# Optimization experiments

Hardware: AMD Instinct MI355X
Metric: run time of the kernel (lower is better)

Reference implementation:

```python
import jax, jax.numpy as jnp
import numpy as np
from jax import lax

B, C, H, W = 8, 64, 96, 96
OC = 64
KH = KW = 3
DG = 1
STRIDE = 1
PAD = 1
DIL = 1


def setup_inputs() -> dict:
    key = jax.random.key(0)
    k1, k2, k3, k4, k5 = jax.random.split(key, 5)
    x = jax.random.normal(k1, (B, C, H, W), jnp.float32)
    off_ch = DG * 3 * KH * KW
    # small random offset/mask conv params (the original inits them to zero,
    # which would make offsets degenerate; small values exercise the sampler)
    w_off = jax.random.normal(k2, (off_ch, C, KH, KW), jnp.float32) * 0.01
    b_off = jax.random.normal(k3, (off_ch,), jnp.float32) * 0.01
    stdv = 1.0 / float(np.sqrt(C * KH * KW))
    weight = jax.random.uniform(k4, (OC, C, KH, KW), jnp.float32, -stdv, stdv)
    bias = jax.random.uniform(k5, (OC,), jnp.float32, -stdv, stdv)
    return {"x": x, "w_off": w_off, "b_off": b_off, "weight": weight, "bias": bias}


def _deform_conv(x, w_off, b_off, weight, bias):
    Bt, Ct, Ht, Wt = x.shape
    K = KH * KW
    # standard conv producing offsets + mask logits
    om = lax.conv_general_dilated(
        x, w_off, (STRIDE, STRIDE), ((PAD, PAD), (PAD, PAD)),
        rhs_dilation=(DIL, DIL), dimension_numbers=("NCHW", "OIHW", "NCHW"),
    ) + b_off[None, :, None, None]
    o1, o2, m = jnp.split(om, 3, axis=1)  # each [B, DG*K, Ho, Wo]
    Ho, Wo = o1.shape[2], o1.shape[3]
    mask = jax.nn.sigmoid(m).reshape(Bt, DG, 1, K, Ho, Wo)
    off_y = o1.reshape(Bt, DG, K, Ho, Wo)
    off_x = o2.reshape(Bt, DG, K, Ho, Wo)
    # base sampling grid: p = out_pos*stride - pad + k*dilation + offset
    kk = jnp.arange(K)
    base_y = (kk // KW)[:, None] * DIL + (jnp.arange(Ho) * STRIDE - PAD)[None, :]  # [K, Ho]
    base_x = (kk % KW)[:, None] * DIL + (jnp.arange(Wo) * STRIDE - PAD)[None, :]   # [K, Wo]
    py = off_y + base_y[None, None, :, :, None].astype(x.dtype)  # [B, DG, K, Ho, Wo]
    px = off_x + base_x[None, None, :, None, :].astype(x.dtype)
    y0 = jnp.floor(py)
    x0 = jnp.floor(px)
    ly = py - y0
    lx = px - x0
    Cg = Ct // DG
    xg = x.reshape(Bt, DG, Cg, Ht * Wt)

    def gath(xf, idx):  # xf [Cg, H*W], idx [K*Ho*Wo]
        return jnp.take(xf, idx, axis=1)

    gather = jax.vmap(jax.vmap(gath))  # over B, DG

    sampled = jnp.zeros((Bt, DG, Cg, K, Ho, Wo), x.dtype)
    for dy, dx, wgt in ((0, 0, (1 - ly) * (1 - lx)), (0, 1, (1 - ly) * lx),
                        (1, 0, ly * (1 - lx)), (1, 1, ly * lx)):
        yy = y0 + dy
        xx = x0 + dx
        valid = (yy >= 0) & (yy < Ht) & (xx >= 0) & (xx < Wt)
        yi = jnp.clip(yy, 0, Ht - 1).astype(jnp.int32)
        xi = jnp.clip(xx, 0, Wt - 1).astype(jnp.int32)
        idx = (yi * Wt + xi).reshape(Bt, DG, K * Ho * Wo)
        v = gather(xg, idx).reshape(Bt, DG, Cg, K, Ho, Wo)
        sampled = sampled + v * (wgt * valid)[:, :, None]
    sampled = sampled * mask  # modulated
    wr = weight.reshape(OC, DG, Cg, K)
    out = jnp.einsum("bgckhw,ogck->bohw", sampled, wr) + bias[None, :, None, None]
    return out


def reference(x, w_off, b_off, weight, bias):
    return _deform_conv(x, w_off, b_off, weight, bias)
```

## Files before the change

### kernel.cpp

```cpp
#include <hip/hip_runtime.h>
#include <math.h>

#define Bn 8
#define Cn 64
#define Hn 96
#define Wn 96
#define HWn (Hn*Wn)
#define OCn 64
#define Kn 9
#define OFFCn 27
#define NPIX (Bn*HWn)
#define PGRPS (NPIX/64)

#define WS_DWORDS (45*NPIX)
#define WS_BYTES  ((size_t)WS_DWORDS*4)

__global__ __launch_bounds__(256, 2) void dcn_k1(
    const float* __restrict__ x,
    const float* __restrict__ w_off,
    const float* __restrict__ b_off,
    float* __restrict__ pwbuf,
    int*   __restrict__ abuf)
{
    __shared__ float lds[4 * 64 * OFFCn];

    const int tid  = threadIdx.x;
    const int lane = tid & 63;
    const int wv   = tid >> 6;
    const int cbase = __builtin_amdgcn_readfirstlane(wv * 16);

    const int p  = blockIdx.x * 64 + lane;
    const int b  = p / HWn;
    const int hw = p % HWn;
    const int ho = hw / Wn;
    const int wo = hw % Wn;

    const float* xb = x + b * (Cn * HWn);

    int   toff[Kn];
    float tval[Kn];
#pragma unroll
    for (int ki = 0; ki < Kn; ++ki) {
        const int yy = ho + ki / 3 - 1, xx = wo + ki % 3 - 1;
        const bool v = (yy >= 0) && (yy < Hn) && (xx >= 0) && (xx < Wn);
        toff[ki] = min(max(yy, 0), Hn - 1) * Wn + min(max(xx, 0), Wn - 1);
        tval[ki] = v ? 1.0f : 0.0f;
    }

    float om[OFFCn];
#pragma unroll
    for (int j = 0; j < OFFCn; ++j) om[j] = 0.0f;

    for (int ci = 0; ci < 16; ++ci) {
        const int c = cbase + ci;
        const float* xc = xb + c * HWn;
        float xk[Kn];
#pragma unroll
        for (int ki = 0; ki < Kn; ++ki)
            xk[ki] = xc[toff[ki]] * tval[ki];

        const float* wc = w_off + c * Kn;
#pragma unroll
        for (int och = 0; och < OFFCn; ++och) {
            const float* wp = wc + och * (Cn * Kn);
            float a = om[och];
#pragma unroll
            for (int ki = 0; ki < Kn; ++ki)
                a = fmaf(xk[ki], wp[ki], a);
            om[och] = a;
        }
    }

#pragma unroll
    for (int j = 0; j < OFFCn; ++j)
        lds[(wv * 64 + lane) * OFFCn + j] = om[j];
    __syncthreads();
#pragma unroll
    for (int j = 0; j < OFFCn; ++j) {
        float a = b_off[j];
#pragma unroll
        for (int ww = 0; ww < 4; ++ww)
            a += lds[(ww * 64 + lane) * OFFCn + j];
        om[j] = a;
    }

    float pw0[Kn], pw1[Kn], pw2[Kn], pw3[Kn];
    int   pav[Kn];
#pragma unroll
    for (int ki = 0; ki < Kn; ++ki) {
        const float py = om[ki]      + (float)(ki / 3 + ho - 1);
        const float px = om[Kn + ki] + (float)(ki % 3 + wo - 1);
        const float m  = 1.0f / (1.0f + __expf(-om[2 * Kn + ki]));

        const float y0f = floorf(py), x0f = floorf(px);
        const float ly = py - y0f, lx = px - x0f;
        const int iy0 = (int)y0f, ix0 = (int)x0f;
        const int iy1 = iy0 + 1,  ix1 = ix0 + 1;

        const float vy0 = (iy0 >= 0 && iy0 < Hn) ? 1.0f : 0.0f;
        const float vy1 = (iy1 >= 0 && iy1 < Hn) ? 1.0f : 0.0f;
        const float vx0 = (ix0 >= 0 && ix0 < Wn) ? 1.0f : 0.0f;
        const float vx1 = (ix1 >= 0 && ix1 < Wn) ? 1.0f : 0.0f;

        const int iy0c = min(max(iy0, 0), Hn - 1);
        const int iy1c = min(max(iy1, 0), Hn - 1);
        const int ix0c = min(max(ix0, 0), Wn - 1);
        const int ix1c = min(max(ix1, 0), Wn - 1);

        pw0[ki] = m * (1.0f - ly) * (1.0f - lx) * vy0 * vx0;
        pw1[ki] = m * (1.0f - ly) * lx          * vy0 * vx1;
        pw2[ki] = m * ly          * (1.0f - lx) * vy1 * vx0;
        pw3[ki] = m * ly          * lx          * vy1 * vx1;
        const int pa  = iy0c * Wn + ix0c;
        const int dx  = ix1c - ix0c;
        const int dyw = (iy1c - iy0c) * Wn;
        pav[ki] = pa | (dx << 16) | (dyw << 17);
    }

    if (wv == 0) {
#pragma unroll
        for (int ki = 0; ki < Kn; ++ki) pwbuf[(0 * Kn + ki) * NPIX + p] = pw0[ki];
#pragma unroll
        for (int ki = 0; ki < Kn; ++ki) abuf[ki * NPIX + p] = pav[ki];
    } else if (wv == 1) {
#pragma unroll
        for (int ki = 0; ki < Kn; ++ki) pwbuf[(1 * Kn + ki) * NPIX + p] = pw1[ki];
    } else if (wv == 2) {
#pragma unroll
        for (int ki = 0; ki < Kn; ++ki) pwbuf[(2 * Kn + ki) * NPIX + p] = pw2[ki];
    } else {
#pragma unroll
        for (int ki = 0; ki < Kn; ++ki) pwbuf[(3 * Kn + ki) * NPIX + p] = pw3[ki];
    }
}

__global__ __launch_bounds__(512, 4) void dcn_k2(
    const float* __restrict__ x,
    const float* __restrict__ weight,
    const float* __restrict__ bias,
    const float* __restrict__ pwbuf,
    const int*   __restrict__ abuf,
    float* __restrict__ out)
{
    __shared__ float smp[8 * Kn * 64];

    const int tid  = threadIdx.x;
    const int lane = tid & 63;
    const int wv   = tid >> 6;
    const int ocb  = __builtin_amdgcn_readfirstlane(wv * 8);

    const int p  = blockIdx.x * 64 + lane;
    const int b  = p / HWn;
    const int hw = p % HWn;

    const float* xb = x + b * (Cn * HWn);

    float pw0[Kn], pw1[Kn], pw2[Kn], pw3[Kn];
    int   pav[Kn];
#pragma unroll
    for (int ki = 0; ki < Kn; ++ki) pw0[ki] = pwbuf[(0 * Kn + ki) * NPIX + p];
#pragma unroll
    for (int ki = 0; ki < Kn; ++ki) pw1[ki] = pwbuf[(1 * Kn + ki) * NPIX + p];
#pragma unroll
    for (int ki = 0; ki < Kn; ++ki) pw2[ki] = pwbuf[(2 * Kn + ki) * NPIX + p];
#pragma unroll
    for (int ki = 0; ki < Kn; ++ki) pw3[ki] = pwbuf[(3 * Kn + ki) * NPIX + p];
#pragma unroll
    for (int ki = 0; ki < Kn; ++ki) pav[ki] = abuf[ki * NPIX + p];

    float acc[8];
#pragma unroll
    for (int j = 0; j < 8; ++j) acc[j] = bias[ocb + j];

    for (int ch = 0; ch < 8; ++ch) {
        {
            const float* xc = xb + (ch * 8 + wv) * HWn;
#pragma unroll
            for (int ki = 0; ki < Kn; ++ki) {
                const int av  = pav[ki];
                const int pa  = av & 0xFFFF;
                const int dx  = (av >> 16) & 1;
                const int dyw = av >> 17;
                const float* bp = xc + pa;
                const float v00 = bp[0];
                const float v01 = bp[dx];
                const float v10 = bp[dyw];
                const float v11 = bp[dyw + dx];
                smp[(wv * Kn + ki) * 64 + lane] =
                    pw0[ki] * v00 + pw1[ki] * v01 + pw2[ki] * v10 + pw3[ki] * v11;
            }
        }
        __syncthreads();

        const float* wch = weight + (ocb * Cn + ch * 8) * Kn;
#pragma unroll 2
        for (int c8 = 0; c8 < 8; ++c8) {
            float sv[Kn];
#pragma unroll
            for (int ki = 0; ki < Kn; ++ki)
                sv[ki] = smp[(c8 * Kn + ki) * 64 + lane];
#pragma unroll
            for (int j = 0; j < 8; ++j) {
                const float* wp = wch + j * (Cn * Kn) + c8 * Kn;
                float a = acc[j];
#pragma unroll
                for (int ki = 0; ki < Kn; ++ki)
                    a = fmaf(sv[ki], wp[ki], a);
                acc[j] = a;
            }
        }
        __syncthreads();
    }

    float* ob = out + b * (OCn * HWn) + hw;
#pragma unroll
    for (int j = 0; j < 8; ++j)
        ob[(ocb + j) * HWn] = acc[j];
}

__global__ __launch_bounds__(64) void dcn_r1(
    const float* __restrict__ x,
    const float* __restrict__ w_off,
    const float* __restrict__ b_off,
    const float* __restrict__ weight,
    const float* __restrict__ bias,
    float* __restrict__ out)
{
    const int p  = blockIdx.x * 64 + threadIdx.x;
    const int b  = p / HWn;
    const int hw = p % HWn;
    const int ho = hw / Wn;
    const int wo = hw % Wn;
    const float* xb = x + b * (Cn * HWn);

    float om[OFFCn];
#pragma unroll
    for (int j = 0; j < OFFCn; ++j) om[j] = b_off[j];

    int   toff[Kn];
    float tval[Kn];
#pragma unroll
    for (int ki = 0; ki < Kn; ++ki) {
        const int yy = ho + ki / 3 - 1, xx = wo + ki % 3 - 1;
        const bool v = (yy >= 0) && (yy < Hn) && (xx >= 0) && (xx < Wn);
        toff[ki] = min(max(yy, 0), Hn - 1) * Wn + min(max(xx, 0), Wn - 1);
        tval[ki] = v ? 1.0f : 0.0f;
    }
    for (int c = 0; c < Cn; ++c) {
        const float* xc = xb + c * HWn;
        float xk[Kn];
#pragma unroll
        for (int ki = 0; ki < Kn; ++ki) xk[ki] = xc[toff[ki]] * tval[ki];
        const float* wc = w_off + c * Kn;
#pragma unroll
        for (int och = 0; och < OFFCn; ++och) {
            const float* wp = wc + och * (Cn * Kn);
            float a = om[och];
#pragma unroll
            for (int ki = 0; ki < Kn; ++ki) a = fmaf(xk[ki], wp[ki], a);
            om[och] = a;
        }
    }
    float pw0[Kn], pw1[Kn], pw2[Kn], pw3[Kn];
    int   pa[Kn], pdx[Kn], pdyw[Kn];
#pragma unroll
    for (int ki = 0; ki < Kn; ++ki) {
        const float py = om[ki]      + (float)(ki / 3 + ho - 1);
        const float px = om[Kn + ki] + (float)(ki % 3 + wo - 1);
        const float m  = 1.0f / (1.0f + __expf(-om[2 * Kn + ki]));
        const float y0f = floorf(py), x0f = floorf(px);
        const float ly = py - y0f, lx = px - x0f;
        const int iy0 = (int)y0f, ix0 = (int)x0f;
        const int iy1 = iy0 + 1,  ix1 = ix0 + 1;
        const float vy0 = (iy0 >= 0 && iy0 < Hn) ? 1.0f : 0.0f;
        const float vy1 = (iy1 >= 0 && iy1 < Hn) ? 1.0f : 0.0f;
        const float vx0 = (ix0 >= 0 && ix0 < Wn) ? 1.0f : 0.0f;
        const float vx1 = (ix1 >= 0 && ix1 < Wn) ? 1.0f : 0.0f;
        const int iy0c = min(max(iy0, 0), Hn - 1);
        const int iy1c = min(max(iy1, 0), Hn - 1);
        const int ix0c = min(max(ix0, 0), Wn - 1);
        const int ix1c = min(max(ix1, 0), Wn - 1);
        pw0[ki] = m * (1.0f - ly) * (1.0f - lx) * vy0 * vx0;
        pw1[ki] = m * (1.0f - ly) * lx          * vy0 * vx1;
        pw2[ki] = m * ly          * (1.0f - lx) * vy1 * vx0;
        pw3[ki] = m * ly          * lx          * vy1 * vx1;
        pa[ki]   = iy0c * Wn + ix0c;
        pdx[ki]  = ix1c - ix0c;
        pdyw[ki] = (iy1c - iy0c) * Wn;
    }
    float acc[OCn];
#pragma unroll
    for (int oc = 0; oc < OCn; ++oc) acc[oc] = bias[oc];
    for (int c = 0; c < Cn; ++c) {
        const float* xc = xb + c * HWn;
        float s[Kn];
#pragma unroll
        for (int ki = 0; ki < Kn; ++ki) {
            const float* bp = xc + pa[ki];
            s[ki] = pw0[ki] * bp[0] + pw1[ki] * bp[pdx[ki]]
                  + pw2[ki] * bp[pdyw[ki]] + pw3[ki] * bp[pdyw[ki] + pdx[ki]];
        }
        const float* wc = weight + c * Kn;
#pragma unroll
        for (int oc = 0; oc < OCn; ++oc) {
            const float* wp = wc + oc * (Cn * Kn);
            float a = acc[oc];
#pragma unroll
            for (int ki = 0; ki < Kn; ++ki) a = fmaf(s[ki], wp[ki], a);
            acc[oc] = a;
        }
    }
    float* ob = out + b * (OCn * HWn) + hw;
#pragma unroll
    for (int oc = 0; oc < OCn; ++oc) ob[oc * HWn] = acc[oc];
}

extern "C" void kernel_launch(void* const* d_in, const int* in_sizes, int n_in,
                              void* d_out, int out_size, void* d_ws, size_t ws_size,
                              hipStream_t stream) {
    const float* x      = (const float*)d_in[0];
    const float* w_off  = (const float*)d_in[1];
    const float* b_off  = (const float*)d_in[2];
    const float* weight = (const float*)d_in[3];
    const float* bias   = (const float*)d_in[4];
    float* out = (float*)d_out;

    if (ws_size >= WS_BYTES) {
        float* pwbuf = (float*)d_ws;
        int*   abuf  = (int*)((float*)d_ws + 36 * NPIX);
        hipLaunchKernelGGL(dcn_k1, dim3(PGRPS), dim3(256), 0, stream,
                           x, w_off, b_off, pwbuf, abuf);
        hipLaunchKernelGGL(dcn_k2, dim3(PGRPS), dim3(512), 0, stream,
                           x, weight, bias, pwbuf, abuf, out);
    } else {
        hipLaunchKernelGGL(dcn_r1, dim3(NPIX / 64), dim3(64), 0, stream,
                           x, w_off, b_off, weight, bias, out);
    }
}
```

Baseline: 283.4 us.

## Move deformable conv GEMM onto bf16 MFMA with split-precision sampled values

Replaces the scalar FMA loop that contracts sampled values against the weights with MFMA 16x16x32 bf16 matrix instructions. A new prep kernel packs the weights into bf16 fragment layout, padded to K=160 per 16-channel chunk. Sampled values are split into high and low bf16 halves, computed on two wave planes, and summed through LDS at the end to keep accuracy close to fp32. The aim is to remove the large VALU FMA cost of the contraction. The trade-offs are an extra launch, padding work, and weights carried only at bf16 precision.

```diff
diff --git a/kernel.cpp b/kernel.cpp
--- a/kernel.cpp
+++ b/kernel.cpp
@@ -12,8 +12,44 @@
 #define NPIX (Bn*HWn)
 #define PGRPS (NPIX/64)
 
-#define WS_DWORDS (45*NPIX)
-#define WS_BYTES  ((size_t)WS_DWORDS*4)
+#define WS_PARAM_DWORDS (45*NPIX)
+#define WPACK_SHORTS (4*20*64*8)
+#define WS_BYTES ((size_t)WS_PARAM_DWORDS*4 + (size_t)WPACK_SHORTS*2)
+
+typedef __attribute__((ext_vector_type(8))) short short8v;
+typedef __attribute__((ext_vector_type(4))) float f32x4;
+
+static __device__ __forceinline__ unsigned short bf16_rne(float f) {
+    unsigned int b = __float_as_uint(f);
+    return (unsigned short)((b + 0x7FFFu + ((b >> 16) & 1u)) >> 16);
+}
+static __device__ __forceinline__ float bf16_back(unsigned short h) {
+    return __uint_as_float(((unsigned int)h) << 16);
+}
+
+__global__ __launch_bounds__(512) void dcn_wprep(
+    const float* __restrict__ weight, short* __restrict__ wpack)
+{
+    const int g = blockIdx.x * 512 + threadIdx.x;
+    const int oct = g / 1280;
+    const int rem = g - oct * 1280;
+    const int gks = rem >> 6;
+    const int l   = rem & 63;
+    const int chunk = gks / 5;
+    const int kk    = (gks % 5) * 32 + ((l >> 4) & 3) * 8;
+    const int oc    = oct * 16 + (l & 15);
+
+    short8v v;
+    if (kk < 144) {
+        const float* src = weight + oc * 576 + chunk * 144 + kk;
+#pragma unroll
+        for (int j = 0; j < 8; ++j) v[j] = (short)bf16_rne(src[j]);
+    } else {
+#pragma unroll
+        for (int j = 0; j < 8; ++j) v[j] = 0;
+    }
+    ((short8v*)wpack)[g] = v;
+}
 
 __global__ __launch_bounds__(256, 2) void dcn_k1(
     const float* __restrict__ x,
@@ -134,24 +170,28 @@
     }
 }
 
+#define SMP_PITCH 66
+#define SMP_U16   (160 * SMP_PITCH)
 __global__ __launch_bounds__(512, 4) void dcn_k2(
     const float* __restrict__ x,
-    const float* __restrict__ weight,
+    const short* __restrict__ wpack,
     const float* __restrict__ bias,
     const float* __restrict__ pwbuf,
     const int*   __restrict__ abuf,
     float* __restrict__ out)
 {
-    __shared__ float smp[8 * Kn * 64];
+    __shared__ unsigned short smp[2 * SMP_U16];
 
     const int tid  = threadIdx.x;
     const int lane = tid & 63;
-    const int wv   = tid >> 6;
-    const int ocb  = __builtin_amdgcn_readfirstlane(wv * 8);
-
-    const int p  = blockIdx.x * 64 + lane;
-    const int b  = p / HWn;
-    const int hw = p % HWn;
+    const int w    = tid >> 6;
+    const int pxt  = w & 3;
+    const int plane= w >> 2;
+
+    const int p0  = blockIdx.x * 64;
+    const int b   = p0 / HWn;
+    const int hwb = p0 % HWn;
+    const int p   = p0 + lane;
 
     const float* xb = x + b * (Cn * HWn);
 
@@ -168,13 +208,26 @@
 #pragma unroll
     for (int ki = 0; ki < Kn; ++ki) pav[ki] = abuf[ki * NPIX + p];
 
-    float acc[8];
-#pragma unroll
-    for (int j = 0; j < 8; ++j) acc[j] = bias[ocb + j];
-
-    for (int ch = 0; ch < 8; ++ch) {
-        {
-            const float* xc = xb + (ch * 8 + wv) * HWn;
+    {
+        unsigned int* zh = (unsigned int*)(smp + 144 * SMP_PITCH);
+        unsigned int* zl = (unsigned int*)(smp + SMP_U16 + 144 * SMP_PITCH);
+        for (int idx = tid; idx < (16 * SMP_PITCH) / 2; idx += 512) {
+            zh[idx] = 0u; zl[idx] = 0u;
+        }
+    }
+
+    f32x4 acc[4];
+#pragma unroll
+    for (int oct = 0; oct < 4; ++oct) acc[oct] = (f32x4){0.f, 0.f, 0.f, 0.f};
+
+    unsigned short* smpP = smp + plane * SMP_U16;
+    const short8v* wfrag = (const short8v*)wpack;
+
+    for (int chunk = 0; chunk < 4; ++chunk) {
+#pragma unroll
+        for (int cc = 0; cc < 2; ++cc) {
+            const int cin = (w << 1) | cc;
+            const float* xc = xb + (chunk * 16 + cin) * HWn;
 #pragma unroll
             for (int ki = 0; ki < Kn; ++ki) {
                 const int av  = pav[ki];
@@ -182,40 +235,63 @@
                 const int dx  = (av >> 16) & 1;
                 const int dyw = av >> 17;
                 const float* bp = xc + pa;
-                const float v00 = bp[0];
-                const float v01 = bp[dx];
-                const float v10 = bp[dyw];
-                const float v11 = bp[dyw + dx];
-                smp[(wv * Kn + ki) * 64 + lane] =
-                    pw0[ki] * v00 + pw1[ki] * v01 + pw2[ki] * v10 + pw3[ki] * v11;
+                const float v = pw0[ki] * bp[0] + pw1[ki] * bp[dx]
+                              + pw2[ki] * bp[dyw] + pw3[ki] * bp[dyw + dx];
+                const unsigned short hb = bf16_rne(v);
+                const unsigned short lb = bf16_rne(v - bf16_back(hb));
+                const int k = cin * Kn + ki;
+                smp[k * SMP_PITCH + lane]            = hb;
+                smp[SMP_U16 + k * SMP_PITCH + lane]  = lb;
             }
         }
         __syncthreads();
 
-        const float* wch = weight + (ocb * Cn + ch * 8) * Kn;
-#pragma unroll 2
-        for (int c8 = 0; c8 < 8; ++c8) {
-            float sv[Kn];
-#pragma unroll
-            for (int ki = 0; ki < Kn; ++ki)
-                sv[ki] = smp[(c8 * Kn + ki) * 64 + lane];
-#pragma unroll
-            for (int j = 0; j < 8; ++j) {
-                const float* wp = wch + j * (Cn * Kn) + c8 * Kn;
-                float a = acc[j];
-#pragma unroll
-                for (int ki = 0; ki < Kn; ++ki)
-                    a = fmaf(sv[ki], wp[ki], a);
-                acc[j] = a;
+#pragma unroll
+        for (int ks = 0; ks < 5; ++ks) {
+            short8v av0 = wfrag[((0 * 20) + chunk * 5 + ks) * 64 + lane];
+            short8v av1 = wfrag[((1 * 20) + chunk * 5 + ks) * 64 + lane];
+            short8v av2 = wfrag[((2 * 20) + chunk * 5 + ks) * 64 + lane];
+            short8v av3 = wfrag[((3 * 20) + chunk * 5 + ks) * 64 + lane];
+
+            short8v bv;
+            const int kb = ks * 32 + ((lane >> 4) & 3) * 8;
+            const int pxl = pxt * 16 + (lane & 15);
+#pragma unroll
+            for (int j = 0; j < 8; ++j)
+                bv[j] = (short)smpP[(kb + j) * SMP_PITCH + pxl];
+
+            acc[0] = __builtin_amdgcn_mfma_f32_16x16x32_bf16(av0, bv, acc[0], 0, 0, 0);
+            acc[1] = __builtin_amdgcn_mfma_f32_16x16x32_bf16(av1, bv, acc[1], 0, 0, 0);
+            acc[2] = __builtin_amdgcn_mfma_f32_16x16x32_bf16(av2, bv, acc[2], 0, 0, 0);
+            acc[3] = __builtin_amdgcn_mfma_f32_16x16x32_bf16(av3, bv, acc[3], 0, 0, 0);
+        }
+        __syncthreads();
+    }
+
+    float* cred = (float*)smp;
+    const int rbase = ((lane >> 4) & 3) * 4;
+    const int pxl   = pxt * 16 + (lane & 15);
+    if (plane == 1) {
+#pragma unroll
+        for (int oct = 0; oct < 4; ++oct)
+#pragma unroll
+            for (int r = 0; r < 4; ++r)
+                cred[(oct * 16 + rbase + r) * SMP_PITCH + pxl] = acc[oct][r];
+    }
+    __syncthreads();
+    if (plane == 0) {
+        float* ob = out + b * (OCn * HWn) + hwb + pxl;
+#pragma unroll
+        for (int oct = 0; oct < 4; ++oct) {
+#pragma unroll
+            for (int r = 0; r < 4; ++r) {
+                const int oc = oct * 16 + rbase + r;
+                const float v = acc[oct][r]
+                              + cred[oc * SMP_PITCH + pxl] + bias[oc];
+                ob[oc * HWn] = v;
             }
         }
-        __syncthreads();
-    }
-
-    float* ob = out + b * (OCn * HWn) + hw;
-#pragma unroll
-    for (int j = 0; j < 8; ++j)
-        ob[(ocb + j) * HWn] = acc[j];
+    }
 }
 
 __global__ __launch_bounds__(64) void dcn_r1(
@@ -328,10 +404,13 @@
     if (ws_size >= WS_BYTES) {
         float* pwbuf = (float*)d_ws;
         int*   abuf  = (int*)((float*)d_ws + 36 * NPIX);
+        short* wpack = (short*)((float*)d_ws + WS_PARAM_DWORDS);
+        hipLaunchKernelGGL(dcn_wprep, dim3(10), dim3(512), 0, stream,
+                           weight, wpack);
         hipLaunchKernelGGL(dcn_k1, dim3(PGRPS), dim3(256), 0, stream,
                            x, w_off, b_off, pwbuf, abuf);
         hipLaunchKernelGGL(dcn_k2, dim3(PGRPS), dim3(512), 0, stream,
-                           x, weight, bias, pwbuf, abuf, out);
+                           x, wpack, bias, pwbuf, abuf, out);
     } else {
         hipLaunchKernelGGL(dcn_r1, dim3(NPIX / 64), dim3(64), 0, stream,
                            x, w_off, b_off, weight, bias, out);
```

New measurement: 418.8 us. +47.8%, slower.

## Convert both kernels to persistent grids with atomic work-stealing over pixel groups

Applied to the files above, without the earlier changes.

Both stages now launch a fixed grid of 1024 blocks that repeatedly pull 64-pixel groups from global atomic counters, which a new tiny kernel zeroes first. The aim is to cut block launch and scheduling overhead and to balance load across CUs. dcn_k1's launch bounds also rise from 2 to 4 blocks per SM to raise occupancy. The cost is an extra kernel launch, one atomic plus a barrier per group, and possible register-pressure effects from the higher occupancy target.

```diff
diff --git a/kernel.cpp b/kernel.cpp
--- a/kernel.cpp
+++ b/kernel.cpp
@@ -12,125 +12,139 @@
 #define NPIX (Bn*HWn)
 #define PGRPS (NPIX/64)
 
-#define WS_DWORDS (45*NPIX)
+#define WS_DWORDS (45*NPIX + 2)
 #define WS_BYTES  ((size_t)WS_DWORDS*4)
 
-__global__ __launch_bounds__(256, 2) void dcn_k1(
+__global__ void dcn_reset(int* __restrict__ cnt) {
+    if (threadIdx.x < 2) cnt[threadIdx.x] = 0;
+}
+
+__global__ __launch_bounds__(256, 4) void dcn_k1(
     const float* __restrict__ x,
     const float* __restrict__ w_off,
     const float* __restrict__ b_off,
     float* __restrict__ pwbuf,
-    int*   __restrict__ abuf)
+    int*   __restrict__ abuf,
+    int*   __restrict__ cnt)
 {
     __shared__ float lds[4 * 64 * OFFCn];
+    __shared__ int sh_g;
 
     const int tid  = threadIdx.x;
     const int lane = tid & 63;
     const int wv   = tid >> 6;
     const int cbase = __builtin_amdgcn_readfirstlane(wv * 16);
 
-    const int p  = blockIdx.x * 64 + lane;
-    const int b  = p / HWn;
-    const int hw = p % HWn;
-    const int ho = hw / Wn;
-    const int wo = hw % Wn;
-
-    const float* xb = x + b * (Cn * HWn);
-
-    int   toff[Kn];
-    float tval[Kn];
-#pragma unroll
-    for (int ki = 0; ki < Kn; ++ki) {
-        const int yy = ho + ki / 3 - 1, xx = wo + ki % 3 - 1;
-        const bool v = (yy >= 0) && (yy < Hn) && (xx >= 0) && (xx < Wn);
-        toff[ki] = min(max(yy, 0), Hn - 1) * Wn + min(max(xx, 0), Wn - 1);
-        tval[ki] = v ? 1.0f : 0.0f;
-    }
-
-    float om[OFFCn];
-#pragma unroll
-    for (int j = 0; j < OFFCn; ++j) om[j] = 0.0f;
-
-    for (int ci = 0; ci < 16; ++ci) {
-        const int c = cbase + ci;
-        const float* xc = xb + c * HWn;
-        float xk[Kn];
-#pragma unroll
-        for (int ki = 0; ki < Kn; ++ki)
-            xk[ki] = xc[toff[ki]] * tval[ki];
-
-        const float* wc = w_off + c * Kn;
-#pragma unroll
-        for (int och = 0; och < OFFCn; ++och) {
-            const float* wp = wc + och * (Cn * Kn);
-            float a = om[och];
+    for (;;) {
+        if (tid == 0) sh_g = atomicAdd(cnt, 1);
+        __syncthreads();
+        const int grp = sh_g;
+        if (grp >= PGRPS) break;
+
+        const int p  = grp * 64 + lane;
+        const int b  = p / HWn;
+        const int hw = p % HWn;
+        const int ho = hw / Wn;
+        const int wo = hw % Wn;
+
+        const float* xb = x + b * (Cn * HWn);
+
+        int   toff[Kn];
+        float tval[Kn];
+#pragma unroll
+        for (int ki = 0; ki < Kn; ++ki) {
+            const int yy = ho + ki / 3 - 1, xx = wo + ki % 3 - 1;
+            const bool v = (yy >= 0) && (yy < Hn) && (xx >= 0) && (xx < Wn);
+            toff[ki] = min(max(yy, 0), Hn - 1) * Wn + min(max(xx, 0), Wn - 1);
+            tval[ki] = v ? 1.0f : 0.0f;
+        }
+
+        float om[OFFCn];
+#pragma unroll
+        for (int j = 0; j < OFFCn; ++j) om[j] = 0.0f;
+
+        for (int ci = 0; ci < 16; ++ci) {
+            const int c = cbase + ci;
+            const float* xc = xb + c * HWn;
+            float xk[Kn];
 #pragma unroll
             for (int ki = 0; ki < Kn; ++ki)
-                a = fmaf(xk[ki], wp[ki], a);
-            om[och] = a;
-        }
-    }
-
-#pragma unroll
-    for (int j = 0; j < OFFCn; ++j)
-        lds[(wv * 64 + lane) * OFFCn + j] = om[j];
-    __syncthreads();
-#pragma unroll
-    for (int j = 0; j < OFFCn; ++j) {
-        float a = b_off[j];
-#pragma unroll
-        for (int ww = 0; ww < 4; ++ww)
-            a += lds[(ww * 64 + lane) * OFFCn + j];
-        om[j] = a;
-    }
-
-    float pw0[Kn], pw1[Kn], pw2[Kn], pw3[Kn];
-    int   pav[Kn];
-#pragma unroll
-    for (int ki = 0; ki < Kn; ++ki) {
-        const float py = om[ki]      + (float)(ki / 3 + ho - 1);
-        const float px = om[Kn + ki] + (float)(ki % 3 + wo - 1);
-        const float m  = 1.0f / (1.0f + __expf(-om[2 * Kn + ki]));
-
-        const float y0f = floorf(py), x0f = floorf(px);
-        const float ly = py - y0f, lx = px - x0f;
-        const int iy0 = (int)y0f, ix0 = (int)x0f;
-        const int iy1 = iy0 + 1,  ix1 = ix0 + 1;
-
-        const float vy0 = (iy0 >= 0 && iy0 < Hn) ? 1.0f : 0.0f;
-        const float vy1 = (iy1 >= 0 && iy1 < Hn) ? 1.0f : 0.0f;
-        const float vx0 = (ix0 >= 0 && ix0 < Wn) ? 1.0f : 0.0f;
-        const float vx1 = (ix1 >= 0 && ix1 < Wn) ? 1.0f : 0.0f;
-
-        const int iy0c = min(max(iy0, 0), Hn - 1);
-        const int iy1c = min(max(iy1, 0), Hn - 1);
-        const int ix0c = min(max(ix0, 0), Wn - 1);
-        const int ix1c = min(max(ix1, 0), Wn - 1);
-
-        pw0[ki] = m * (1.0f - ly) * (1.0f - lx) * vy0 * vx0;
-        pw1[ki] = m * (1.0f - ly) * lx          * vy0 * vx1;
-        pw2[ki] = m * ly          * (1.0f - lx) * vy1 * vx0;
-        pw3[ki] = m * ly          * lx          * vy1 * vx1;
-        const int pa  = iy0c * Wn + ix0c;
-        const int dx  = ix1c - ix0c;
-        const int dyw = (iy1c - iy0c) * Wn;
-        pav[ki] = pa | (dx << 16) | (dyw << 17);
-    }
-
-    if (wv == 0) {
-#pragma unroll
-        for (int ki = 0; ki < Kn; ++ki) pwbuf[(0 * Kn + ki) * NPIX + p] = pw0[ki];
-#pragma unroll
-        for (int ki = 0; ki < Kn; ++ki) abuf[ki * NPIX + p] = pav[ki];
-    } else if (wv == 1) {
-#pragma unroll
-        for (int ki = 0; ki < Kn; ++ki) pwbuf[(1 * Kn + ki) * NPIX + p] = pw1[ki];
-    } else if (wv == 2) {
-#pragma unroll
-        for (int ki = 0; ki < Kn; ++ki) pwbuf[(2 * Kn + ki) * NPIX + p] = pw2[ki];
-    } else {
-#pragma unroll
-        for (int ki = 0; ki < Kn; ++ki) pwbuf[(3 * Kn + ki) * NPIX + p] = pw3[ki];
+                xk[ki] = xc[toff[ki]] * tval[ki];
+
+            const float* wc = w_off + c * Kn;
+#pragma unroll
+            for (int och = 0; och < OFFCn; ++och) {
+                const float* wp = wc + och * (Cn * Kn);
+                float a = om[och];
+#pragma unroll
+                for (int ki = 0; ki < Kn; ++ki)
+                    a = fmaf(xk[ki], wp[ki], a);
+                om[och] = a;
+            }
+        }
+
+#pragma unroll
+        for (int j = 0; j < OFFCn; ++j)
+            lds[(wv * 64 + lane) * OFFCn + j] = om[j];
+        __syncthreads();
+#pragma unroll
+        for (int j = 0; j < OFFCn; ++j) {
+            float a = b_off[j];
+#pragma unroll
+            for (int ww = 0; ww < 4; ++ww)
+                a += lds[(ww * 64 + lane) * OFFCn + j];
+            om[j] = a;
+        }
+
+        float pw0[Kn], pw1[Kn], pw2[Kn], pw3[Kn];
+        int   pav[Kn];
+#pragma unroll
+        for (int ki = 0; ki < Kn; ++ki) {
+            const float py = om[ki]      + (float)(ki / 3 + ho - 1);
+            const float px = om[Kn + ki] + (float)(ki % 3 + wo - 1);
+            const float m  = 1.0f / (1.0f + __expf(-om[2 * Kn + ki]));
+
+            const float y0f = floorf(py), x0f = floorf(px);
+            const float ly = py - y0f, lx = px - x0f;
+            const int iy0 = (int)y0f, ix0 = (int)x0f;
+            const int iy1 = iy0 + 1,  ix1 = ix0 + 1;
+
+            const float vy0 = (iy0 >= 0 && iy0 < Hn) ? 1.0f : 0.0f;
+            const float vy1 = (iy1 >= 0 && iy1 < Hn) ? 1.0f : 0.0f;
+            const float vx0 = (ix0 >= 0 && ix0 < Wn) ? 1.0f : 0.0f;
+            const float vx1 = (ix1 >= 0 && ix1 < Wn) ? 1.0f : 0.0f;
+
+            const int iy0c = min(max(iy0, 0), Hn - 1);
+            const int iy1c = min(max(iy1, 0), Hn - 1);
+            const int ix0c = min(max(ix0, 0), Wn - 1);
+            const int ix1c = min(max(ix1, 0), Wn - 1);
+
+            pw0[ki] = m * (1.0f - ly) * (1.0f - lx) * vy0 * vx0;
+            pw1[ki] = m * (1.0f - ly) * lx          * vy0 * vx1;
+            pw2[ki] = m * ly          * (1.0f - lx) * vy1 * vx0;
+            pw3[ki] = m * ly          * lx          * vy1 * vx1;
+            const int pa  = iy0c * Wn + ix0c;
+            const int dx  = ix1c - ix0c;
+            const int dyw = (iy1c - iy0c) * Wn;
+            pav[ki] = pa | (dx << 16) | (dyw << 17);
+        }
+
+        if (wv == 0) {
+#pragma unroll
+            for (int ki = 0; ki < Kn; ++ki) pwbuf[(0 * Kn + ki) * NPIX + p] = pw0[ki];
+#pragma unroll
+            for (int ki = 0; ki < Kn; ++ki) abuf[ki * NPIX + p] = pav[ki];
+        } else if (wv == 1) {
+#pragma unroll
+            for (int ki = 0; ki < Kn; ++ki) pwbuf[(1 * Kn + ki) * NPIX + p] = pw1[ki];
+        } else if (wv == 2) {
+#pragma unroll
+            for (int ki = 0; ki < Kn; ++ki) pwbuf[(2 * Kn + ki) * NPIX + p] = pw2[ki];
+        } else {
+#pragma unroll
+            for (int ki = 0; ki < Kn; ++ki) pwbuf[(3 * Kn + ki) * NPIX + p] = pw3[ki];
+        }
+        __syncthreads();
     }
 }
 
@@ -140,82 +154,91 @@
     const float* __restrict__ bias,
     const float* __restrict__ pwbuf,
     const int*   __restrict__ abuf,
+    int*   __restrict__ cnt,
     float* __restrict__ out)
 {
     __shared__ float smp[8 * Kn * 64];
+    __shared__ int sh_g;
 
     const int tid  = threadIdx.x;
     const int lane = tid & 63;
     const int wv   = tid >> 6;
     const int ocb  = __builtin_amdgcn_readfirstlane(wv * 8);
 
-    const int p  = blockIdx.x * 64 + lane;
-    const int b  = p / HWn;
-    const int hw = p % HWn;
-
-    const float* xb = x + b * (Cn * HWn);
-
-    float pw0[Kn], pw1[Kn], pw2[Kn], pw3[Kn];
-    int   pav[Kn];
-#pragma unroll
-    for (int ki = 0; ki < Kn; ++ki) pw0[ki] = pwbuf[(0 * Kn + ki) * NPIX + p];
-#pragma unroll
-    for (int ki = 0; ki < Kn; ++ki) pw1[ki] = pwbuf[(1 * Kn + ki) * NPIX + p];
-#pragma unroll
-    for (int ki = 0; ki < Kn; ++ki) pw2[ki] = pwbuf[(2 * Kn + ki) * NPIX + p];
-#pragma unroll
-    for (int ki = 0; ki < Kn; ++ki) pw3[ki] = pwbuf[(3 * Kn + ki) * NPIX + p];
-#pragma unroll
-    for (int ki = 0; ki < Kn; ++ki) pav[ki] = abuf[ki * NPIX + p];
-
-    float acc[8];
-#pragma unroll
-    for (int j = 0; j < 8; ++j) acc[j] = bias[ocb + j];
-
-    for (int ch = 0; ch < 8; ++ch) {
-        {
-            const float* xc = xb + (ch * 8 + wv) * HWn;
-#pragma unroll
-            for (int ki = 0; ki < Kn; ++ki) {
-                const int av  = pav[ki];
-                const int pa  = av & 0xFFFF;
-                const int dx  = (av >> 16) & 1;
-                const int dyw = av >> 17;
-                const float* bp = xc + pa;
-                const float v00 = bp[0];
-                const float v01 = bp[dx];
-                const float v10 = bp[dyw];
-                const float v11 = bp[dyw + dx];
-                smp[(wv * Kn + ki) * 64 + lane] =
-                    pw0[ki] * v00 + pw1[ki] * v01 + pw2[ki] * v10 + pw3[ki] * v11;
+    for (;;) {
+        if (tid == 0) sh_g = atomicAdd(cnt + 1, 1);
+        __syncthreads();
+        const int grp = sh_g;
+        if (grp >= PGRPS) break;
+
+        const int p  = grp * 64 + lane;
+        const int b  = p / HWn;
+        const int hw = p % HWn;
+
+        const float* xb = x + b * (Cn * HWn);
+
+        float pw0[Kn], pw1[Kn], pw2[Kn], pw3[Kn];
+        int   pav[Kn];
+#pragma unroll
+        for (int ki = 0; ki < Kn; ++ki) pw0[ki] = pwbuf[(0 * Kn + ki) * NPIX + p];
+#pragma unroll
+        for (int ki = 0; ki < Kn; ++ki) pw1[ki] = pwbuf[(1 * Kn + ki) * NPIX + p];
+#pragma unroll
+        for (int ki = 0; ki < Kn; ++ki) pw2[ki] = pwbuf[(2 * Kn + ki) * NPIX + p];
+#pragma unroll
+        for (int ki = 0; ki < Kn; ++ki) pw3[ki] = pwbuf[(3 * Kn + ki) * NPIX + p];
+#pragma unroll
+        for (int ki = 0; ki < Kn; ++ki) pav[ki] = abuf[ki * NPIX + p];
+
+        float acc[8];
+#pragma unroll
+        for (int j = 0; j < 8; ++j) acc[j] = bias[ocb + j];
+
+        for (int ch = 0; ch < 8; ++ch) {
+            {
+                const float* xc = xb + (ch * 8 + wv) * HWn;
+#pragma unroll
+                for (int ki = 0; ki < Kn; ++ki) {
+                    const int av  = pav[ki];
+                    const int pa  = av & 0xFFFF;
+                    const int dx  = (av >> 16) & 1;
+                    const int dyw = av >> 17;
+                    const float* bp = xc + pa;
+                    const float v00 = bp[0];
+                    const float v01 = bp[dx];
+                    const float v10 = bp[dyw];
+                    const float v11 = bp[dyw + dx];
+                    smp[(wv * Kn + ki) * 64 + lane] =
+                        pw0[ki] * v00 + pw1[ki] * v01 + pw2[ki] * v10 + pw3[ki] * v11;
+                }
             }
-        }
-        __syncthreads();
-
-        const float* wch = weight + (ocb * Cn + ch * 8) * Kn;
+            __syncthreads();
+
+            const float* wch = weight + (ocb * Cn + ch * 8) * Kn;
 #pragma unroll 2
-        for (int c8 = 0; c8 < 8; ++c8) {
-            float sv[Kn];
-#pragma unroll
-            for (int ki = 0; ki < Kn; ++ki)
-                sv[ki] = smp[(c8 * Kn + ki) * 64 + lane];
-#pragma unroll
-            for (int j = 0; j < 8; ++j) {
-                const float* wp = wch + j * (Cn * Kn) + c8 * Kn;
-                float a = acc[j];
+            for (int c8 = 0; c8 < 8; ++c8) {
+                float sv[Kn];
 #pragma unroll
                 for (int ki = 0; ki < Kn; ++ki)
-                    a = fmaf(sv[ki], wp[ki], a);
-                acc[j] = a;
+                    sv[ki] = smp[(c8 * Kn + ki) * 64 + lane];
+#pragma unroll
+                for (int j = 0; j < 8; ++j) {
+                    const float* wp = wch + j * (Cn * Kn) + c8 * Kn;
+                    float a = acc[j];
+#pragma unroll
+                    for (int ki = 0; ki < Kn; ++ki)
+                        a = fmaf(sv[ki], wp[ki], a);
+                    acc[j] = a;
+                }
             }
-        }
-        __syncthreads();
-    }
-
-    float* ob = out + b * (OCn * HWn) + hw;
-#pragma unroll
-    for (int j = 0; j < 8; ++j)
-        ob[(ocb + j) * HWn] = acc[j];
+            __syncthreads();
+        }
+
+        float* ob = out + b * (OCn * HWn) + hw;
+#pragma unroll
+        for (int j = 0; j < 8; ++j)
+            ob[(ocb + j) * HWn] = acc[j];
+    }
 }
 
 __global__ __launch_bounds__(64) void dcn_r1(
@@ -328,10 +351,12 @@
     if (ws_size >= WS_BYTES) {
         float* pwbuf = (float*)d_ws;
         int*   abuf  = (int*)((float*)d_ws + 36 * NPIX);
-        hipLaunchKernelGGL(dcn_k1, dim3(PGRPS), dim3(256), 0, stream,
-                           x, w_off, b_off, pwbuf, abuf);
-        hipLaunchKernelGGL(dcn_k2, dim3(PGRPS), dim3(512), 0, stream,
-                           x, weight, bias, pwbuf, abuf, out);
+        int*   cnt   = (int*)((float*)d_ws + 45 * NPIX);
+        hipLaunchKernelGGL(dcn_reset, dim3(1), dim3(64), 0, stream, cnt);
+        hipLaunchKernelGGL(dcn_k1, dim3(1024), dim3(256), 0, stream,
+                           x, w_off, b_off, pwbuf, abuf, cnt);
+        hipLaunchKernelGGL(dcn_k2, dim3(1024), dim3(512), 0, stream,
+                           x, weight, bias, pwbuf, abuf, cnt, out);
     } else {
         hipLaunchKernelGGL(dcn_r1, dim3(NPIX / 64), dim3(64), 0, stream,
                            x, w_off, b_off, weight, bias, out);
```

New measurement: 312.1 us. 10.1% more time.

## Prepack conv weights into contiguous streams and widen k2 channel chunks

Applied to the files above, without the earlier changes.

Adds a small prep kernel that repacks the offset-conv and main-conv weights so each wave reads its weights as one contiguous, wave-uniform stream instead of strided scalar loads. In dcn_k2 the channel chunk grows from 8 to 16 per barrier pair, with each wave sampling two channels, which halves the number of __syncthreads iterations. The LDS buffer doubles in size, which may reduce occupancy, and there is an extra kernel launch plus more workspace.

```diff
diff --git a/kernel.cpp b/kernel.cpp
--- a/kernel.cpp
+++ b/kernel.cpp
@@ -12,12 +12,40 @@
 #define NPIX (Bn*HWn)
 #define PGRPS (NPIX/64)
 
-#define WS_DWORDS (45*NPIX)
+#define WPK1_N 15552
+#define WPK2_N 36864
+#define WS_DWORDS (45*NPIX + WPK1_N + WPK2_N)
 #define WS_BYTES  ((size_t)WS_DWORDS*4)
+
+__global__ __launch_bounds__(256) void dcn_wprep(
+    const float* __restrict__ w_off,
+    const float* __restrict__ weight,
+    float* __restrict__ wpk1,
+    float* __restrict__ wpk2)
+{
+    const int g = blockIdx.x * 256 + threadIdx.x;
+    if (g < WPK1_N) {
+        const int c_all = g / 243;
+        const int och   = (g % 243) / 9;
+        const int ki    = g % 9;
+        wpk1[g] = w_off[(och * 64 + c_all) * 9 + ki];
+    }
+    const int h = g - WPK1_N;
+    if (h >= 0 && h < WPK2_N) {
+        const int ki  = h % 9;
+        const int j   = (h / 9) % 8;
+        const int c16 = (h / 72) % 16;
+        const int ch  = (h / 1152) % 4;
+        const int wv  = h / 4608;
+        const int oc  = wv * 8 + j;
+        const int c   = ch * 16 + c16;
+        wpk2[h] = weight[(oc * 64 + c) * 9 + ki];
+    }
+}
 
 __global__ __launch_bounds__(256, 2) void dcn_k1(
     const float* __restrict__ x,
-    const float* __restrict__ w_off,
+    const float* __restrict__ wpk1,
     const float* __restrict__ b_off,
     float* __restrict__ pwbuf,
     int*   __restrict__ abuf)
@@ -51,18 +79,18 @@
 #pragma unroll
     for (int j = 0; j < OFFCn; ++j) om[j] = 0.0f;
 
+    const float* wstream = wpk1 + cbase * 243;
     for (int ci = 0; ci < 16; ++ci) {
-        const int c = cbase + ci;
-        const float* xc = xb + c * HWn;
+        const float* xc = xb + (cbase + ci) * HWn;
         float xk[Kn];
 #pragma unroll
         for (int ki = 0; ki < Kn; ++ki)
             xk[ki] = xc[toff[ki]] * tval[ki];
 
-        const float* wc = w_off + c * Kn;
+        const float* wc = wstream + ci * 243;
 #pragma unroll
         for (int och = 0; och < OFFCn; ++och) {
-            const float* wp = wc + och * (Cn * Kn);
+            const float* wp = wc + och * 9;
             float a = om[och];
 #pragma unroll
             for (int ki = 0; ki < Kn; ++ki)
@@ -136,13 +164,13 @@
 
 __global__ __launch_bounds__(512, 4) void dcn_k2(
     const float* __restrict__ x,
-    const float* __restrict__ weight,
+    const float* __restrict__ wpk2,
     const float* __restrict__ bias,
     const float* __restrict__ pwbuf,
     const int*   __restrict__ abuf,
     float* __restrict__ out)
 {
-    __shared__ float smp[8 * Kn * 64];
+    __shared__ float smp[16 * Kn * 64];
 
     const int tid  = threadIdx.x;
     const int lane = tid & 63;
@@ -172,9 +200,13 @@
 #pragma unroll
     for (int j = 0; j < 8; ++j) acc[j] = bias[ocb + j];
 
-    for (int ch = 0; ch < 8; ++ch) {
-        {
-            const float* xc = xb + (ch * 8 + wv) * HWn;
+    const float* wbase = wpk2 + __builtin_amdgcn_readfirstlane(wv * 4 * 1152);
+
+    for (int ch = 0; ch < 4; ++ch) {
+#pragma unroll
+        for (int cc = 0; cc < 2; ++cc) {
+            const int cin = (wv << 1) | cc;
+            const float* xc = xb + (ch * 16 + cin) * HWn;
 #pragma unroll
             for (int ki = 0; ki < Kn; ++ki) {
                 const int av  = pav[ki];
@@ -186,22 +218,23 @@
                 const float v01 = bp[dx];
                 const float v10 = bp[dyw];
                 const float v11 = bp[dyw + dx];
-                smp[(wv * Kn + ki) * 64 + lane] =
+                smp[(cin * Kn + ki) * 64 + lane] =
                     pw0[ki] * v00 + pw1[ki] * v01 + pw2[ki] * v10 + pw3[ki] * v11;
             }
         }
         __syncthreads();
 
-        const float* wch = weight + (ocb * Cn + ch * 8) * Kn;
+        const float* ws2 = wbase + ch * 1152;
 #pragma unroll 2
-        for (int c8 = 0; c8 < 8; ++c8) {
+        for (int c16 = 0; c16 < 16; ++c16) {
             float sv[Kn];
 #pragma unroll
             for (int ki = 0; ki < Kn; ++ki)
-                sv[ki] = smp[(c8 * Kn + ki) * 64 + lane];
+                sv[ki] = smp[(c16 * Kn + ki) * 64 + lane];
+            const float* wc = ws2 + c16 * 72;
 #pragma unroll
             for (int j = 0; j < 8; ++j) {
-                const float* wp = wch + j * (Cn * Kn) + c8 * Kn;
+                const float* wp = wc + j * 9;
                 float a = acc[j];
 #pragma unroll
                 for (int ki = 0; ki < Kn; ++ki)
@@ -328,10 +361,14 @@
     if (ws_size >= WS_BYTES) {
         float* pwbuf = (float*)d_ws;
         int*   abuf  = (int*)((float*)d_ws + 36 * NPIX);
+        float* wpk1  = (float*)d_ws + 45 * NPIX;
+        float* wpk2  = wpk1 + WPK1_N;
+        hipLaunchKernelGGL(dcn_wprep, dim3((WPK1_N + WPK2_N + 255) / 256), dim3(256),
+                           0, stream, w_off, weight, wpk1, wpk2);
         hipLaunchKernelGGL(dcn_k1, dim3(PGRPS), dim3(256), 0, stream,
-                           x, w_off, b_off, pwbuf, abuf);
+                           x, wpk1, b_off, pwbuf, abuf);
         hipLaunchKernelGGL(dcn_k2, dim3(PGRPS), dim3(512), 0, stream,
-                           x, weight, bias, pwbuf, abuf, out);
+                           x, wpk2, bias, pwbuf, abuf, out);
     } else {
         hipLaunchKernelGGL(dcn_r1, dim3(NPIX / 64), dim3(64), 0, stream,
                            x, w_off, b_off, weight, bias, out);
```

Result: faster. 256.7 us (-9.4%).
